# Kernel tuning notes

Measured on AMD Instinct MI355X. Metric: run time of the kernel, lower is better.

## Reference

```python
import jax, jax.numpy as jnp
import numpy as np

D = 1024
HEADS = 16
LN_EPS = 1e-5   # torch LayerNorm default
SHEP_EPS = 1e-4 # eps in shepards_MHA
SHEP_P = 2


def setup_inputs() -> dict:
    key = jax.random.key(0)
    k1, k2, k3 = jax.random.split(key, 3)
    b, t, d = 2, 2048, D
    X = jax.random.normal(k1, (b, t, d), dtype=jnp.float32)
    # Linear weights, scaled like torch default init (~U(-1/sqrt(fan_in), ...)) magnitude
    W_in = jax.random.normal(k2, (4 * d, d), dtype=jnp.float32) * (1.0 / np.sqrt(d))
    b_in = jnp.zeros((4 * d,), dtype=jnp.float32)
    W_out = jax.random.normal(k3, (d, d), dtype=jnp.float32) * (1.0 / np.sqrt(d))
    b_out = jnp.zeros((d,), dtype=jnp.float32)
    return {"X": X, "W_in": W_in, "b_in": b_in, "W_out": W_out, "b_out": b_out}


def _shepards_mha(Q, K, V):
    # Q,K,V: [b,h,t,dh]. Euclidean cdist via ||q||^2 + ||k||^2 - 2 q.k
    q2 = jnp.sum(Q * Q, axis=-1, keepdims=True)          # [b,h,t,1]
    k2 = jnp.sum(K * K, axis=-1, keepdims=True)          # [b,h,t,1]
    sq = q2 + jnp.swapaxes(k2, -1, -2) - 2.0 * jnp.einsum('bhqd,bhkd->bhqk', Q, K)
    dist = jnp.sqrt(jnp.maximum(sq, 0.0))                # [b,h,t,t]
    W = (SHEP_EPS + dist) ** (-SHEP_P)
    W = W / (SHEP_EPS + jnp.sum(W, axis=-1, keepdims=True))
    return jnp.einsum('bhqk,bhkd->bhqd', W, V)


def reference(X, W_in, b_in, W_out, b_out):
    b, t, d = X.shape
    h = HEADS
    dh = d // h
    # LayerNorm (no affine)
    mu = jnp.mean(X, axis=-1, keepdims=True)
    var = jnp.mean((X - mu) ** 2, axis=-1, keepdims=True)
    Xn = (X - mu) / jnp.sqrt(var + LN_EPS)
    # project_in: [b,t,4d]
    P = jnp.einsum('btd,ed->bte', Xn, W_in) + b_in
    # [b,t,h,4*dh] -> [b,h,t,4*dh]
    P = P.reshape(b, t, h, 4 * dh).transpose(0, 2, 1, 3)
    Q, K, V, G = jnp.split(P, 4, axis=-1)                # each [b,h,t,dh]
    A = _shepards_mha(Q, K, V)
    O = (G * A).transpose(0, 2, 1, 3).reshape(b, t, d)
    return X + jnp.einsum('btd,ed->bte', O, W_out) + b_out
```

## Files before the change

### kernel.cpp

```cpp
#include <hip/hip_runtime.h>

#define SEQ 2048
#define D_MODEL 1024
#define NTOK 4096
#define PROW 4096
#define DH 64
#define LN_EPS 1e-5f
#define SHEP_EPS 1e-4f

typedef __attribute__((ext_vector_type(8))) short bf16x8;
typedef __attribute__((ext_vector_type(4))) short s16x4;
typedef __attribute__((ext_vector_type(4))) float f32x4;

__device__ __forceinline__ unsigned short f2bf(float f) {
  union { float f; unsigned u; } v; v.f = f;
  unsigned r = v.u + 0x7fffu + ((v.u >> 16) & 1u);
  return (unsigned short)(r >> 16);
}
__device__ __forceinline__ float bf2f(unsigned short s) {
  union { unsigned u; float f; } v; v.u = ((unsigned)s) << 16;
  return v.f;
}
__device__ __forceinline__ void gload16(const void* g, void* l) {
  __builtin_amdgcn_global_load_lds(
      (const __attribute__((address_space(1))) unsigned int*)g,
      (__attribute__((address_space(3))) unsigned int*)l, 16, 0, 0);
}
__device__ __forceinline__ void gload4(const void* g, void* l) {
  __builtin_amdgcn_global_load_lds(
      (const __attribute__((address_space(1))) unsigned int*)g,
      (__attribute__((address_space(3))) unsigned int*)l, 4, 0, 0);
}
__device__ __forceinline__ unsigned cvt_pk_bf16(float lo, float hi) {
  unsigned r;
  asm("v_cvt_pk_bf16_f32 %0, %1, %2" : "=v"(r) : "v"(lo), "v"(hi));
  return r;
}
#define MFMA16(a, b, c) __builtin_amdgcn_mfma_f32_16x16x32_bf16(a, b, c, 0, 0, 0)

__global__ __launch_bounds__(256) void ln_kernel(const float* __restrict__ X,
                                                 unsigned short* __restrict__ Xn) {
  int row = blockIdx.x, tid = threadIdx.x;
  const float4* xr = (const float4*)(X + (size_t)row * D_MODEL);
  float4 v = xr[tid];
  float s = v.x + v.y + v.z + v.w;
  float s2 = v.x * v.x + v.y * v.y + v.z * v.z + v.w * v.w;
#pragma unroll
  for (int off = 32; off > 0; off >>= 1) {
    s += __shfl_down(s, off);
    s2 += __shfl_down(s2, off);
  }
  __shared__ float red[8];
  __shared__ float mb[2];
  int wv = tid >> 6;
  if ((tid & 63) == 0) { red[wv] = s; red[4 + wv] = s2; }
  __syncthreads();
  if (tid == 0) {
    float ts = red[0] + red[1] + red[2] + red[3];
    float t2 = red[4] + red[5] + red[6] + red[7];
    float mu = ts * (1.f / D_MODEL);
    float var = t2 * (1.f / D_MODEL) - mu * mu;
    mb[0] = mu;
    mb[1] = rsqrtf(var + LN_EPS);
  }
  __syncthreads();
  float mu = mb[0], rs = mb[1];
  s16x4 o;
  o[0] = (short)f2bf((v.x - mu) * rs);
  o[1] = (short)f2bf((v.y - mu) * rs);
  o[2] = (short)f2bf((v.z - mu) * rs);
  o[3] = (short)f2bf((v.w - mu) * rs);
  ((s16x4*)(Xn + (size_t)row * D_MODEL))[tid] = o;
}

__global__ __launch_bounds__(256) void cvt_bf16_kernel(const float* __restrict__ in,
                                                       unsigned short* __restrict__ out,
                                                       int n4) {
  int i = blockIdx.x * 256 + threadIdx.x;
  if (i >= n4) return;
  float4 v = ((const float4*)in)[i];
  s16x4 o;
  o[0] = (short)f2bf(v.x);
  o[1] = (short)f2bf(v.y);
  o[2] = (short)f2bf(v.z);
  o[3] = (short)f2bf(v.w);
  ((s16x4*)out)[i] = o;
}

__global__ __launch_bounds__(256) void gemm_p_kernel(
    const unsigned short* __restrict__ A, const unsigned short* __restrict__ B,
    const float* __restrict__ bias, unsigned short* __restrict__ C,
    int M, int N, int K) {
  __shared__ __align__(16) unsigned short sA[128 * 32];
  __shared__ __align__(16) unsigned short sB[128 * 32];
  int tid = threadIdx.x;
  int m0 = blockIdx.y * 128, n0 = blockIdx.x * 128;
  int wv = tid >> 6, lane = tid & 63;
  int wr = wv >> 1, wc = wv & 1;
  int lr = lane & 15, lq = lane >> 4;
  f32x4 acc[4][4] = {};
  int srow = tid >> 2, scol = (tid & 3) * 8;
  const unsigned short* gA = A + (size_t)(m0 + srow) * K + scol;
  const unsigned short* gB = B + (size_t)(n0 + srow) * K + scol;
  unsigned short* lA = sA + tid * 8;
  unsigned short* lB = sB + tid * 8;
  for (int k0 = 0; k0 < K; k0 += 32) {
    gload16(gA + k0, lA);
    gload16(gA + k0 + (size_t)64 * K, lA + 64 * 32);
    gload16(gB + k0, lB);
    gload16(gB + k0 + (size_t)64 * K, lB + 64 * 32);
    __syncthreads();
    bf16x8 af[4], bfr[4];
#pragma unroll
    for (int m = 0; m < 4; m++)
      af[m] = *(const bf16x8*)&sA[(wr * 64 + m * 16 + lr) * 32 + lq * 8];
#pragma unroll
    for (int n = 0; n < 4; n++)
      bfr[n] = *(const bf16x8*)&sB[(wc * 64 + n * 16 + lr) * 32 + lq * 8];
#pragma unroll
    for (int m = 0; m < 4; m++)
#pragma unroll
      for (int n = 0; n < 4; n++)
        acc[m][n] = MFMA16(af[m], bfr[n], acc[m][n]);
    __syncthreads();
  }
#pragma unroll
  for (int m = 0; m < 4; m++) {
    int row = m0 + wr * 64 + m * 16 + lq * 4;
#pragma unroll
    for (int n = 0; n < 4; n++) {
      int col = n0 + wc * 64 + n * 16 + lr;
      float bv = bias[col];
#pragma unroll
      for (int r = 0; r < 4; r++)
        C[(size_t)(row + r) * N + col] = f2bf(acc[m][n][r] + bv);
    }
  }
}

__global__ __launch_bounds__(256) void gemm_out_kernel(
    const unsigned short* __restrict__ A, const unsigned short* __restrict__ B,
    const float* __restrict__ bias, const float* __restrict__ Xres,
    float* __restrict__ Out, int M, int N, int K) {
  __shared__ __align__(16) unsigned short sA[128 * 32];
  __shared__ __align__(16) unsigned short sB[128 * 32];
  int tid = threadIdx.x;
  int m0 = blockIdx.y * 128, n0 = blockIdx.x * 128;
  int wv = tid >> 6, lane = tid & 63;
  int wr = wv >> 1, wc = wv & 1;
  int lr = lane & 15, lq = lane >> 4;
  f32x4 acc[4][4] = {};
  int srow = tid >> 2, scol = (tid & 3) * 8;
  const unsigned short* gA = A + (size_t)(m0 + srow) * K + scol;
  const unsigned short* gB = B + (size_t)(n0 + srow) * K + scol;
  unsigned short* lA = sA + tid * 8;
  unsigned short* lB = sB + tid * 8;
  for (int k0 = 0; k0 < K; k0 += 32) {
    gload16(gA + k0, lA);
    gload16(gA + k0 + (size_t)64 * K, lA + 64 * 32);
    gload16(gB + k0, lB);
    gload16(gB + k0 + (size_t)64 * K, lB + 64 * 32);
    __syncthreads();
    bf16x8 af[4], bfr[4];
#pragma unroll
    for (int m = 0; m < 4; m++)
      af[m] = *(const bf16x8*)&sA[(wr * 64 + m * 16 + lr) * 32 + lq * 8];
#pragma unroll
    for (int n = 0; n < 4; n++)
      bfr[n] = *(const bf16x8*)&sB[(wc * 64 + n * 16 + lr) * 32 + lq * 8];
#pragma unroll
    for (int m = 0; m < 4; m++)
#pragma unroll
      for (int n = 0; n < 4; n++)
        acc[m][n] = MFMA16(af[m], bfr[n], acc[m][n]);
    __syncthreads();
  }
#pragma unroll
  for (int m = 0; m < 4; m++) {
    int row = m0 + wr * 64 + m * 16 + lq * 4;
#pragma unroll
    for (int n = 0; n < 4; n++) {
      int col = n0 + wc * 64 + n * 16 + lr;
      float bv = bias[col];
#pragma unroll
      for (int r = 0; r < 4; r++) {
        size_t idx = (size_t)(row + r) * N + col;
        Out[idx] = Xres[idx] + acc[m][n][r] + bv;
      }
    }
  }
}

__global__ __launch_bounds__(256) void transv_kernel(const unsigned short* __restrict__ P,
                                                     unsigned short* __restrict__ Vt) {
  int kt = blockIdx.x;
  int bh = blockIdx.y;
  int b = bh >> 4, h = bh & 15;
  __shared__ unsigned short sT[64][72];
  int tid = threadIdx.x;
  const unsigned short* vbase = P + ((size_t)(b * SEQ + kt * 64)) * PROW + h * 256 + 128;
#pragma unroll
  for (int it = 0; it < 2; it++) {
    int c = tid + it * 256;
    int k = c >> 3, c0 = (c & 7) * 8;
    uint4 u = *(const uint4*)(vbase + (size_t)k * PROW + c0);
    unsigned e[4] = {u.x, u.y, u.z, u.w};
#pragma unroll
    for (int j = 0; j < 4; j++) {
      sT[c0 + 2 * j][k] = (unsigned short)(e[j] & 0xffffu);
      sT[c0 + 2 * j + 1][k] = (unsigned short)(e[j] >> 16);
    }
  }
  __syncthreads();
  unsigned short* obase = Vt + (size_t)bh * 64 * SEQ + kt * 64;
#pragma unroll
  for (int it = 0; it < 2; it++) {
    int cc = tid + it * 256;
    int crow = cc >> 3, k0 = (cc & 7) * 8;
    uint4 o;
    unsigned short e[8];
#pragma unroll
    for (int j = 0; j < 8; j++) e[j] = sT[crow][k0 + j];
    o.x = (unsigned)e[0] | ((unsigned)e[1] << 16);
    o.y = (unsigned)e[2] | ((unsigned)e[3] << 16);
    o.z = (unsigned)e[4] | ((unsigned)e[5] << 16);
    o.w = (unsigned)e[6] | ((unsigned)e[7] << 16);
    *(uint4*)(obase + (size_t)crow * SEQ + k0) = o;
  }
}

__global__ __launch_bounds__(256) void norms_kernel(const unsigned short* __restrict__ P,
                                                    float* __restrict__ nrm) {
  int id = blockIdx.x * 256 + threadIdx.x;
  int bh = id >> 12;
  int which = (id >> 11) & 1;
  int t = id & 2047;
  int b = bh >> 4, h = bh & 15;
  const unsigned short* p = P + ((size_t)(b * SEQ + t)) * PROW + h * 256 + which * 64;
  const uint4* pv = (const uint4*)p;
  float acc = 0.f;
#pragma unroll
  for (int i = 0; i < 8; i++) {
    uint4 u = pv[i];
    unsigned arr[4] = {u.x, u.y, u.z, u.w};
#pragma unroll
    for (int j = 0; j < 4; j++) {
      float lo = __uint_as_float(arr[j] << 16);
      float hi = __uint_as_float(arr[j] & 0xffff0000u);
      acc += lo * lo + hi * hi;
    }
  }
  nrm[(size_t)(bh * 2 + which) * SEQ + t] = acc;
}

__global__ __launch_bounds__(256) void attn_kernel(
    const unsigned short* __restrict__ P, const unsigned short* __restrict__ Vt,
    const float* __restrict__ nrm, unsigned short* __restrict__ O) {
  const int NT = SEQ / 64;
  int qt = blockIdx.x, bh = blockIdx.y;
  int b = bh >> 4, h = bh & 15;
  int tid = threadIdx.x;
  int w = tid >> 6, lane = tid & 63;
  int lr = lane & 15, lq = lane >> 4;

  __shared__ __align__(16) unsigned short sQ[128 * 64];
  __shared__ __align__(16) unsigned short sK[2][64 * 64];
  __shared__ __align__(16) unsigned short sV[2][64 * 64];
  __shared__ __align__(16) unsigned short sW[128 * 64];
  __shared__ __align__(16) float sK2[2][64];
  __shared__ __align__(16) float sDen[4][2][16];

  const unsigned short* qbase = P + ((size_t)(b * SEQ + qt * 128)) * PROW + h * 256;
  const unsigned short* kbase = P + ((size_t)(b * SEQ)) * PROW + h * 256 + 64;
  const unsigned short* vtb = Vt + (size_t)bh * 64 * SEQ;
  const float* k2base = nrm + (size_t)(bh * 2 + 1) * SEQ;

  auto stage_kv = [&](int t, int buf) {
#pragma unroll
    for (int it = 0; it < 2; it++) {
      int c = tid + it * 256;
      int row = c >> 3;
      int col = ((c & 7) ^ (row & 7)) * 8;
      gload16(kbase + (size_t)(t * 64 + row) * PROW + col, (char*)&sK[buf][0] + c * 16);
      gload16(vtb + (size_t)row * SEQ + t * 64 + col, (char*)&sV[buf][0] + c * 16);
    }
    if (tid < 64) gload4(k2base + t * 64 + tid, (char*)&sK2[buf][0] + tid * 4);
  };

#pragma unroll
  for (int it = 0; it < 4; it++) {
    int c = tid + it * 256;
    int row = c >> 3;
    int col = ((c & 7) ^ (row & 7)) * 8;
    gload16(qbase + (size_t)row * PROW + col, (char*)sQ + c * 16);
  }
  stage_kv(0, 0);
  float q2f0 = nrm[(size_t)(bh * 2) * SEQ + qt * 128 + 32 * w + lr];
  float q2f1 = nrm[(size_t)(bh * 2) * SEQ + qt * 128 + 32 * w + 16 + lr];
  __syncthreads();

  bf16x8 qf[2][2];
#pragma unroll
  for (int fq = 0; fq < 2; fq++) {
    int row = 32 * w + 16 * fq + lr;
#pragma unroll
    for (int ks = 0; ks < 2; ks++)
      qf[fq][ks] = *(const bf16x8*)((const char*)sQ + row * 128 +
                                    ((ks * 64 + lq * 16) ^ ((row & 7) << 4)));
  }

  f32x4 num[2][4] = {};
  float den[2] = {0.f, 0.f};
  char* wrow0 = (char*)sW + (32 * w + lr) * 128;
  char* wrow1 = (char*)sW + (32 * w + 16 + lr) * 128;

  for (int t = 0; t < NT; t++) {
    int cur = t & 1;
    if (t + 1 < NT) stage_kv(t + 1, cur ^ 1);

    f32x4 st[2][4] = {};
    __builtin_amdgcn_s_setprio(1);
#pragma unroll
    for (int fk = 0; fk < 4; fk++) {
      int row = 16 * fk + lr;
      const char* krow = (const char*)&sK[cur][0] + row * 128;
      bf16x8 kf0 = *(const bf16x8*)(krow + ((lq * 16) ^ ((row & 7) << 4)));
      bf16x8 kf1 = *(const bf16x8*)(krow + ((64 + lq * 16) ^ ((row & 7) << 4)));
      st[0][fk] = MFMA16(kf0, qf[0][0], st[0][fk]);
      st[0][fk] = MFMA16(kf1, qf[0][1], st[0][fk]);
      st[1][fk] = MFMA16(kf0, qf[1][0], st[1][fk]);
      st[1][fk] = MFMA16(kf1, qf[1][1], st[1][fk]);
    }
    __builtin_amdgcn_s_setprio(0);

#pragma unroll
    for (int fk = 0; fk < 4; fk++) {
      f32x4 k2v = *(const f32x4*)&sK2[cur][16 * fk + 4 * lq];
#pragma unroll
      for (int fq = 0; fq < 2; fq++) {
        float q2 = fq ? q2f1 : q2f0;
        float w0 = __builtin_amdgcn_rcpf(fmaxf(fmaf(-2.f, st[fq][fk][0], q2 + k2v[0]), 1e-8f));
        float w1 = __builtin_amdgcn_rcpf(fmaxf(fmaf(-2.f, st[fq][fk][1], q2 + k2v[1]), 1e-8f));
        float w2 = __builtin_amdgcn_rcpf(fmaxf(fmaf(-2.f, st[fq][fk][2], q2 + k2v[2]), 1e-8f));
        float w3 = __builtin_amdgcn_rcpf(fmaxf(fmaf(-2.f, st[fq][fk][3], q2 + k2v[3]), 1e-8f));
        den[fq] += (w0 + w1) + (w2 + w3);
        uint2 pp;
        pp.x = cvt_pk_bf16(w0, w1);
        pp.y = cvt_pk_bf16(w2, w3);
        char* wr = fq ? wrow1 : wrow0;
        *(uint2*)(wr + ((32 * fk + 8 * lq) ^ ((lr & 7) << 4))) = pp;
      }
    }

    __builtin_amdgcn_s_setprio(1);
#pragma unroll
    for (int ks = 0; ks < 2; ks++) {
      bf16x8 aw0 = *(const bf16x8*)(wrow0 + ((64 * ks + 16 * lq) ^ ((lr & 7) << 4)));
      bf16x8 aw1 = *(const bf16x8*)(wrow1 + ((64 * ks + 16 * lq) ^ ((lr & 7) << 4)));
#pragma unroll
      for (int fn = 0; fn < 4; fn++) {
        int row = 16 * fn + lr;
        bf16x8 bv = *(const bf16x8*)((const char*)&sV[cur][0] + row * 128 +
                                     ((64 * ks + 16 * lq) ^ ((row & 7) << 4)));
        num[0][fn] = MFMA16(aw0, bv, num[0][fn]);
        num[1][fn] = MFMA16(aw1, bv, num[1][fn]);
      }
    }
    __builtin_amdgcn_s_setprio(0);

    __syncthreads();
  }

#pragma unroll
  for (int fq = 0; fq < 2; fq++) {
    den[fq] += __shfl_xor(den[fq], 16);
    den[fq] += __shfl_xor(den[fq], 32);
  }
  if (lq == 0) {
    sDen[w][0][lr] = den[0];
    sDen[w][1][lr] = den[1];
  }
  __syncthreads();

  const unsigned short* gbase = qbase + 192;
#pragma unroll
  for (int fq = 0; fq < 2; fq++) {
    f32x4 dv = *(const f32x4*)&sDen[w][fq][4 * lq];
    f32x4 rdv;
#pragma unroll
    for (int r = 0; r < 4; r++)
      rdv[r] = __builtin_amdgcn_rcpf(dv[r] + SHEP_EPS);
#pragma unroll
    for (int fn = 0; fn < 4; fn++) {
      int c = 16 * fn + lr;
#pragma unroll
      for (int r = 0; r < 4; r++) {
        int ql = 32 * w + 16 * fq + 4 * lq + r;
        float g = bf2f(gbase[(size_t)ql * PROW + c]);
        O[((size_t)(b * SEQ + qt * 128 + ql)) * D_MODEL + h * DH + c] =
            f2bf(g * num[fq][fn][r] * rdv[r]);
      }
    }
  }
}

extern "C" void kernel_launch(void* const* d_in, const int* in_sizes, int n_in,
                              void* d_out, int out_size, void* d_ws, size_t ws_size,
                              hipStream_t stream) {
  const float* X = (const float*)d_in[0];
  const float* W_in = (const float*)d_in[1];
  const float* b_in = (const float*)d_in[2];
  const float* W_out = (const float*)d_in[3];
  const float* b_out = (const float*)d_in[4];
  float* out = (float*)d_out;

  char* ws = (char*)d_ws;
  unsigned short* Xn = (unsigned short*)(ws);
  unsigned short* O = (unsigned short*)(ws);
  unsigned short* Wi = (unsigned short*)(ws + ((size_t)8 << 20));
  unsigned short* Vt = (unsigned short*)(ws + ((size_t)8 << 20));
  unsigned short* Wo = (unsigned short*)(ws + ((size_t)16 << 20));
  unsigned short* P = (unsigned short*)(ws + ((size_t)18 << 20));
  float* nrm = (float*)(ws + ((size_t)50 << 20));

  ln_kernel<<<NTOK, 256, 0, stream>>>(X, Xn);
  cvt_bf16_kernel<<<4096, 256, 0, stream>>>(W_in, Wi, (4096 * 1024) / 4);
  cvt_bf16_kernel<<<1024, 256, 0, stream>>>(W_out, Wo, (1024 * 1024) / 4);
  gemm_p_kernel<<<dim3(32, 32), 256, 0, stream>>>(Xn, Wi, b_in, P, 4096, 4096, 1024);
  transv_kernel<<<dim3(32, 32), 256, 0, stream>>>(P, Vt);
  norms_kernel<<<512, 256, 0, stream>>>(P, nrm);
  attn_kernel<<<dim3(16, 32), 256, 0, stream>>>(P, Vt, nrm, O);
  gemm_out_kernel<<<dim3(8, 32), 256, 0, stream>>>(O, Wo, b_out, X, out, 4096, 1024, 1024);
}
```

Baseline: 173.9 us.

## Widen GEMM K-tiles with swizzled LDS, XCD-swizzle blocks, deepen attention prefetch, fuse weight casts

The two GEMMs now stage 64-wide K tiles into XOR-swizzled LDS, which halves the number of barriers per K and avoids bank conflicts. They also remap workgroups so neighbouring tiles land on the same XCD for L2 reuse. The attention loop prefetches two KV tiles ahead, using explicit vmcnt waits and raw s_barrier instead of __syncthreads. The two weight-cast launches are merged into one kernel that writes Wi and Wo contiguously, relying on Wo sitting right after Wi in the workspace (8 MB + 8 MB = 16 MB offset). The hand-tuned vmcnt counts are fragile if the compiler reorders or changes the number of loads.

```diff
diff --git a/kernel.cpp b/kernel.cpp
--- a/kernel.cpp
+++ b/kernel.cpp
@@ -37,6 +37,11 @@
   return r;
 }
 #define MFMA16(a, b, c) __builtin_amdgcn_mfma_f32_16x16x32_bf16(a, b, c, 0, 0, 0)
+
+__device__ __forceinline__ int xcd_swizzle(int linear, int nwg) {
+  int cpx = nwg >> 3;
+  return (linear & 7) * cpx + (linear >> 3);
+}
 
 __global__ __launch_bounds__(256) void ln_kernel(const float* __restrict__ X,
                                                  unsigned short* __restrict__ Xn) {
@@ -73,55 +78,67 @@
   ((s16x4*)(Xn + (size_t)row * D_MODEL))[tid] = o;
 }
 
-__global__ __launch_bounds__(256) void cvt_bf16_kernel(const float* __restrict__ in,
-                                                       unsigned short* __restrict__ out,
-                                                       int n4) {
+__global__ __launch_bounds__(256) void cvt_both_kernel(const float* __restrict__ Win,
+                                                       const float* __restrict__ Wout,
+                                                       unsigned short* __restrict__ dst) {
+  const int N1 = (4096 * 1024) / 4;
+  const int N2 = (1024 * 1024) / 4;
   int i = blockIdx.x * 256 + threadIdx.x;
-  if (i >= n4) return;
-  float4 v = ((const float4*)in)[i];
+  if (i >= N1 + N2) return;
+  float4 v = (i < N1) ? ((const float4*)Win)[i] : ((const float4*)Wout)[i - N1];
   s16x4 o;
   o[0] = (short)f2bf(v.x);
   o[1] = (short)f2bf(v.y);
   o[2] = (short)f2bf(v.z);
   o[3] = (short)f2bf(v.w);
-  ((s16x4*)out)[i] = o;
+  ((s16x4*)dst)[i] = o;
 }
 
 __global__ __launch_bounds__(256) void gemm_p_kernel(
     const unsigned short* __restrict__ A, const unsigned short* __restrict__ B,
     const float* __restrict__ bias, unsigned short* __restrict__ C,
     int M, int N, int K) {
-  __shared__ __align__(16) unsigned short sA[128 * 32];
-  __shared__ __align__(16) unsigned short sB[128 * 32];
+  __shared__ __align__(16) unsigned short sA[128 * 64];
+  __shared__ __align__(16) unsigned short sB[128 * 64];
   int tid = threadIdx.x;
-  int m0 = blockIdx.y * 128, n0 = blockIdx.x * 128;
+  int nwg = gridDim.x * gridDim.y;
+  int swz = xcd_swizzle(blockIdx.y * gridDim.x + blockIdx.x, nwg);
+  int m0 = (swz / gridDim.x) * 128, n0 = (swz % gridDim.x) * 128;
   int wv = tid >> 6, lane = tid & 63;
   int wr = wv >> 1, wc = wv & 1;
   int lr = lane & 15, lq = lane >> 4;
   f32x4 acc[4][4] = {};
-  int srow = tid >> 2, scol = (tid & 3) * 8;
-  const unsigned short* gA = A + (size_t)(m0 + srow) * K + scol;
-  const unsigned short* gB = B + (size_t)(n0 + srow) * K + scol;
-  unsigned short* lA = sA + tid * 8;
-  unsigned short* lB = sB + tid * 8;
-  for (int k0 = 0; k0 < K; k0 += 32) {
-    gload16(gA + k0, lA);
-    gload16(gA + k0 + (size_t)64 * K, lA + 64 * 32);
-    gload16(gB + k0, lB);
-    gload16(gB + k0 + (size_t)64 * K, lB + 64 * 32);
+  for (int k0 = 0; k0 < K; k0 += 64) {
+#pragma unroll
+    for (int it = 0; it < 4; it++) {
+      int c = tid + it * 256;
+      int row = c >> 3;
+      int col = ((c & 7) ^ (row & 7)) * 8;
+      gload16(A + (size_t)(m0 + row) * K + k0 + col, (char*)sA + c * 16);
+      gload16(B + (size_t)(n0 + row) * K + k0 + col, (char*)sB + c * 16);
+    }
     __syncthreads();
-    bf16x8 af[4], bfr[4];
-#pragma unroll
-    for (int m = 0; m < 4; m++)
-      af[m] = *(const bf16x8*)&sA[(wr * 64 + m * 16 + lr) * 32 + lq * 8];
-#pragma unroll
-    for (int n = 0; n < 4; n++)
-      bfr[n] = *(const bf16x8*)&sB[(wc * 64 + n * 16 + lr) * 32 + lq * 8];
-#pragma unroll
-    for (int m = 0; m < 4; m++)
-#pragma unroll
-      for (int n = 0; n < 4; n++)
-        acc[m][n] = MFMA16(af[m], bfr[n], acc[m][n]);
+#pragma unroll
+    for (int ks = 0; ks < 2; ks++) {
+      bf16x8 af[4], bfr[4];
+#pragma unroll
+      for (int m = 0; m < 4; m++) {
+        int row = wr * 64 + m * 16 + lr;
+        af[m] = *(const bf16x8*)((const char*)sA + row * 128 +
+                                 (((ks * 4 + lq) ^ (lr & 7)) * 16));
+      }
+#pragma unroll
+      for (int n = 0; n < 4; n++) {
+        int row = wc * 64 + n * 16 + lr;
+        bfr[n] = *(const bf16x8*)((const char*)sB + row * 128 +
+                                  (((ks * 4 + lq) ^ (lr & 7)) * 16));
+      }
+#pragma unroll
+      for (int m = 0; m < 4; m++)
+#pragma unroll
+        for (int n = 0; n < 4; n++)
+          acc[m][n] = MFMA16(af[m], bfr[n], acc[m][n]);
+    }
     __syncthreads();
   }
 #pragma unroll
@@ -142,37 +159,47 @@
     const unsigned short* __restrict__ A, const unsigned short* __restrict__ B,
     const float* __restrict__ bias, const float* __restrict__ Xres,
     float* __restrict__ Out, int M, int N, int K) {
-  __shared__ __align__(16) unsigned short sA[128 * 32];
-  __shared__ __align__(16) unsigned short sB[128 * 32];
+  __shared__ __align__(16) unsigned short sA[128 * 64];
+  __shared__ __align__(16) unsigned short sB[128 * 64];
   int tid = threadIdx.x;
-  int m0 = blockIdx.y * 128, n0 = blockIdx.x * 128;
+  int nwg = gridDim.x * gridDim.y;
+  int swz = xcd_swizzle(blockIdx.y * gridDim.x + blockIdx.x, nwg);
+  int m0 = (swz / gridDim.x) * 128, n0 = (swz % gridDim.x) * 128;
   int wv = tid >> 6, lane = tid & 63;
   int wr = wv >> 1, wc = wv & 1;
   int lr = lane & 15, lq = lane >> 4;
   f32x4 acc[4][4] = {};
-  int srow = tid >> 2, scol = (tid & 3) * 8;
-  const unsigned short* gA = A + (size_t)(m0 + srow) * K + scol;
-  const unsigned short* gB = B + (size_t)(n0 + srow) * K + scol;
-  unsigned short* lA = sA + tid * 8;
-  unsigned short* lB = sB + tid * 8;
-  for (int k0 = 0; k0 < K; k0 += 32) {
-    gload16(gA + k0, lA);
-    gload16(gA + k0 + (size_t)64 * K, lA + 64 * 32);
-    gload16(gB + k0, lB);
-    gload16(gB + k0 + (size_t)64 * K, lB + 64 * 32);
+  for (int k0 = 0; k0 < K; k0 += 64) {
+#pragma unroll
+    for (int it = 0; it < 4; it++) {
+      int c = tid + it * 256;
+      int row = c >> 3;
+      int col = ((c & 7) ^ (row & 7)) * 8;
+      gload16(A + (size_t)(m0 + row) * K + k0 + col, (char*)sA + c * 16);
+      gload16(B + (size_t)(n0 + row) * K + k0 + col, (char*)sB + c * 16);
+    }
     __syncthreads();
-    bf16x8 af[4], bfr[4];
-#pragma unroll
-    for (int m = 0; m < 4; m++)
-      af[m] = *(const bf16x8*)&sA[(wr * 64 + m * 16 + lr) * 32 + lq * 8];
-#pragma unroll
-    for (int n = 0; n < 4; n++)
-      bfr[n] = *(const bf16x8*)&sB[(wc * 64 + n * 16 + lr) * 32 + lq * 8];
-#pragma unroll
-    for (int m = 0; m < 4; m++)
-#pragma unroll
-      for (int n = 0; n < 4; n++)
-        acc[m][n] = MFMA16(af[m], bfr[n], acc[m][n]);
+#pragma unroll
+    for (int ks = 0; ks < 2; ks++) {
+      bf16x8 af[4], bfr[4];
+#pragma unroll
+      for (int m = 0; m < 4; m++) {
+        int row = wr * 64 + m * 16 + lr;
+        af[m] = *(const bf16x8*)((const char*)sA + row * 128 +
+                                 (((ks * 4 + lq) ^ (lr & 7)) * 16));
+      }
+#pragma unroll
+      for (int n = 0; n < 4; n++) {
+        int row = wc * 64 + n * 16 + lr;
+        bfr[n] = *(const bf16x8*)((const char*)sB + row * 128 +
+                                  (((ks * 4 + lq) ^ (lr & 7)) * 16));
+      }
+#pragma unroll
+      for (int m = 0; m < 4; m++)
+#pragma unroll
+        for (int n = 0; n < 4; n++)
+          acc[m][n] = MFMA16(af[m], bfr[n], acc[m][n]);
+    }
     __syncthreads();
   }
 #pragma unroll
@@ -295,8 +322,10 @@
     gload16(qbase + (size_t)row * PROW + col, (char*)sQ + c * 16);
   }
   stage_kv(0, 0);
+  stage_kv(1, 1);
   float q2f0 = nrm[(size_t)(bh * 2) * SEQ + qt * 128 + 32 * w + lr];
   float q2f1 = nrm[(size_t)(bh * 2) * SEQ + qt * 128 + 32 * w + 16 + lr];
+  asm volatile("" ::"v"(q2f0), "v"(q2f1));
   __syncthreads();
 
   bf16x8 qf[2][2];
@@ -316,7 +345,15 @@
 
   for (int t = 0; t < NT; t++) {
     int cur = t & 1;
-    if (t + 1 < NT) stage_kv(t + 1, cur ^ 1);
+    if (t == NT - 1)
+      asm volatile("s_waitcnt vmcnt(0)" ::: "memory");
+    else if (w == 0)
+      asm volatile("s_waitcnt vmcnt(5)" ::: "memory");
+    else
+      asm volatile("s_waitcnt vmcnt(4)" ::: "memory");
+    __builtin_amdgcn_sched_barrier(0);
+    __builtin_amdgcn_s_barrier();
+    __builtin_amdgcn_sched_barrier(0);
 
     f32x4 st[2][4] = {};
     __builtin_amdgcn_s_setprio(1);
@@ -368,7 +405,10 @@
     }
     __builtin_amdgcn_s_setprio(0);
 
-    __syncthreads();
+    __builtin_amdgcn_sched_barrier(0);
+    __builtin_amdgcn_s_barrier();
+    __builtin_amdgcn_sched_barrier(0);
+    if (t + 2 < NT) stage_kv(t + 2, cur);
   }
 
 #pragma unroll
@@ -424,8 +464,7 @@
   float* nrm = (float*)(ws + ((size_t)50 << 20));
 
   ln_kernel<<<NTOK, 256, 0, stream>>>(X, Xn);
-  cvt_bf16_kernel<<<4096, 256, 0, stream>>>(W_in, Wi, (4096 * 1024) / 4);
-  cvt_bf16_kernel<<<1024, 256, 0, stream>>>(W_out, Wo, (1024 * 1024) / 4);
+  cvt_both_kernel<<<5120, 256, 0, stream>>>(W_in, W_out, Wi);
   gemm_p_kernel<<<dim3(32, 32), 256, 0, stream>>>(Xn, Wi, b_in, P, 4096, 4096, 1024);
   transv_kernel<<<dim3(32, 32), 256, 0, stream>>>(P, Vt);
   norms_kernel<<<512, 256, 0, stream>>>(P, nrm);
```

Result: faster. 153.9 us (-11.5%).
